# Kernel optimization log

Measured on AMD Instinct MI355X. Metric: run time of the kernel, lower is better.

The kernel has to match this reference:

```python
import jax, jax.numpy as jnp
import numpy as np

N, D_IN, D_OUT, H = 8192, 256, 128, 2
SLOPE = 0.2
EPS = 1e-5  # InstanceNorm2d default eps


def setup_inputs() -> dict:
    key = jax.random.key(0)
    ks = jax.random.split(key, 6)
    x = jax.random.normal(ks[0], (N, D_IN), dtype=jnp.float32)
    conn_mask = jnp.where(jax.random.uniform(ks[1], (N, N)) < 0.05, 0.0, -1e9).astype(jnp.float32)
    W = jax.random.normal(ks[2], (H, D_IN, D_OUT), dtype=jnp.float32) * 0.05
    a_src = jax.random.normal(ks[3], (H, D_OUT), dtype=jnp.float32) * 0.1
    a_tgt = jax.random.normal(ks[4], (H, D_OUT), dtype=jnp.float32) * 0.1
    W_res = jax.random.normal(ks[5], (D_OUT, D_IN), dtype=jnp.float32) * 0.05
    return {"x": x, "conn_mask": conn_mask, "W": W, "a_src": a_src, "a_tgt": a_tgt, "W_res": W_res}


def reference(x, conn_mask, W, a_src, a_tgt, W_res):
    # dropout is identity in eval mode
    proj = jnp.einsum('nd,hdf->hnf', x, W)                      # [H,N,F]
    s_src = jnp.einsum('hnf,hf->hn', proj, a_src)[:, :, None]   # [H,N,1]
    s_tgt = jnp.einsum('hnf,hf->hn', proj, a_tgt)[:, None, :]   # [H,1,N]
    scores = jax.nn.leaky_relu(s_src + s_tgt, negative_slope=SLOPE)  # [H,N,N]
    attn = jax.nn.softmax(conn_mask[None] + scores, axis=1)     # softmax over dim=1 as in torch code
    vals = jnp.einsum('hmn,hnf->hmf', attn, proj)               # bmm -> [H,N,F]
    vals = vals.mean(axis=0)                                    # head mean -> [N,F]
    # InstanceNorm2d(1, affine=False) over the whole [N,F] plane, biased variance
    mu = vals.mean()
    var = jnp.mean(jnp.square(vals - mu))
    vals_norm = (vals - mu) / jnp.sqrt(var + EPS)
    out = vals_norm + x @ W_res.T                               # residual projection (no bias)
    out = jax.nn.elu(out)
    return (out, conn_mask)
```

## Files before the change

kernel.cpp:

```cpp
#include <hip/hip_runtime.h>
#include <stdint.h>

#define NN   8192
#define DIN  256
#define FF   128
#define NF   (NN*FF)
#define SLOPE 0.2f
#define EPSI  1e-5f
#define LOG2E 1.4426950408889634f
#define GEMMB 256

typedef short bf16x8 __attribute__((ext_vector_type(8)));
typedef float f32x4 __attribute__((ext_vector_type(4)));

#define OFF_BM     0
#define OFF_RESID  (2*NF)
#define OFF_AVEC   (3*NF)
#define OFF_SS     (4*NF)
#define OFF_ST     (OFF_SS + 2*NN)
#define OFF_CSUM   (OFF_ST + 2*NN)
#define OFF_STATS  (OFF_CSUM + 2*NN)
#define OFF_NTAB   (OFF_STATS + 16)
#define OFF_VALS   (OFF_NTAB + 4*NN)
#define OFF_WT     (OFF_VALS + NF)
#define OFF_PT2    (OFF_WT + DIN*FF)
#define OFF_VPART  (OFF_PT2 + NF)

__device__ __forceinline__ float lrelu(float x) { return x >= 0.f ? x : SLOPE * x; }

__device__ __forceinline__ float exp2fast(float x) { return __builtin_amdgcn_exp2f(x); }

__device__ __forceinline__ uint32_t bfpack(float a, float b) {
  uint32_t ua = __float_as_uint(a); ua += 0x7fffu + ((ua >> 16) & 1u);
  uint32_t ub = __float_as_uint(b); ub += 0x7fffu + ((ub >> 16) & 1u);
  return (ua >> 16) | (ub & 0xffff0000u);
}

__global__ __launch_bounds__(256) void k_prep(const float* __restrict__ wres, float* __restrict__ wtr,
                                              const float* __restrict__ W, const float* __restrict__ a_src,
                                              const float* __restrict__ a_tgt, float* __restrict__ avec) {
  const int b = blockIdx.x;
  if (b < 128) {
    int i = b * 256 + threadIdx.x;
    int d = i >> 7, f = i & 127;
    wtr[i] = wres[f * DIN + d];
  } else {
    int j = b - 128;
    int h = j & 1, tg = j >> 1;
    const float* a = (tg ? a_tgt : a_src) + h * FF;
    const float* Wp = W + ((size_t)h * DIN + threadIdx.x) * FF;
    float s = 0.f;
#pragma unroll 8
    for (int f = 0; f < FF; ++f) s += Wp[f] * a[f];
    avec[j * DIN + threadIdx.x] = s;
  }
}

__global__ __launch_bounds__(256) void k_ss(const float* __restrict__ x, const float* __restrict__ avec,
                                            float* __restrict__ ss, float* __restrict__ st) {
  const int lane = threadIdx.x & 63, wid = threadIdx.x >> 6;
  const int n = blockIdx.x * 4 + wid;
  float4 xv = *(const float4*)&x[n * DIN + 4 * lane];
  float4 c0 = *(const float4*)&avec[0 * DIN + 4 * lane];
  float4 c1 = *(const float4*)&avec[1 * DIN + 4 * lane];
  float4 c2 = *(const float4*)&avec[2 * DIN + 4 * lane];
  float4 c3 = *(const float4*)&avec[3 * DIN + 4 * lane];
  float v0 = xv.x * c0.x + xv.y * c0.y + xv.z * c0.z + xv.w * c0.w;
  float v1 = xv.x * c1.x + xv.y * c1.y + xv.z * c1.z + xv.w * c1.w;
  float v2 = xv.x * c2.x + xv.y * c2.y + xv.z * c2.z + xv.w * c2.w;
  float v3 = xv.x * c3.x + xv.y * c3.y + xv.z * c3.z + xv.w * c3.w;
#pragma unroll
  for (int o = 1; o < 64; o <<= 1) {
    v0 += __shfl_xor(v0, o); v1 += __shfl_xor(v1, o);
    v2 += __shfl_xor(v2, o); v3 += __shfl_xor(v3, o);
  }
  if (lane == 0) { ss[n] = v0; ss[NN + n] = v1; st[n] = v2; st[NN + n] = v3; }
}

__global__ __launch_bounds__(256) void k_fused(const float* __restrict__ mask, float* __restrict__ maskout,
                                               const float* __restrict__ ss, const float* __restrict__ st,
                                               float* __restrict__ csum, uint32_t* __restrict__ bitmask,
                                               const float* __restrict__ x, const float* __restrict__ Wh,
                                               const float* __restrict__ wtr, uint32_t* __restrict__ pt2,
                                               float* __restrict__ resid) {
  __shared__ float xs[32 * 68];
  __shared__ uint32_t pw[32][129];
  const int b = blockIdx.x;
  const int tid = threadIdx.x;

  if (b >= GEMMB) {
    const int bc = b - GEMMB;
    const int bx = bc & 31, by = bc >> 5;
    const int lane = tid & 63, wv = tid >> 6;
    const int n = bx * 256 + tid;
    const int m0 = by * 128;
    const int wbase = bx * 8 + wv * 2;
    const float st0 = st[n] * LOG2E, st1 = st[NN + n] * LOG2E;
    const float ssA = ss[m0 + lane] * LOG2E,      ssB = ss[m0 + 64 + lane] * LOG2E;
    const float ssC = ss[NN + m0 + lane] * LOG2E, ssD = ss[NN + m0 + 64 + lane] * LOG2E;
    float c0 = 0.f, c1 = 0.f;

    for (int i = 0; i < 128; i += 8) {
      float v[8];
#pragma unroll
      for (int r = 0; r < 8; ++r)
        v[r] = __builtin_nontemporal_load(&mask[(size_t)(m0 + i + r) * NN + n]);
#pragma unroll
      for (int r = 0; r < 8; ++r) {
        const int m = m0 + i + r;
        __builtin_nontemporal_store(v[r], &maskout[(size_t)m * NN + n]);
        bool e = v[r] > -0.5e9f;
        unsigned long long bm = __ballot(e);
        if (lane == 0)
          *(uint2*)&bitmask[m * 256 + wbase] = make_uint2((uint32_t)bm, (uint32_t)(bm >> 32));
        const int ri = i + r;
        float s0 = __uint_as_float(__builtin_amdgcn_readlane(
                     __float_as_uint(ri < 64 ? ssA : ssB), ri & 63));
        float s1 = __uint_as_float(__builtin_amdgcn_readlane(
                     __float_as_uint(ri < 64 ? ssC : ssD), ri & 63));
        float w0 = exp2fast(lrelu(s0 + st0));
        float w1 = exp2fast(lrelu(s1 + st1));
        c0 += e ? w0 : 0.f;
        c1 += e ? w1 : 0.f;
      }
    }
    atomicAdd(&csum[n], c0);
    atomicAdd(&csum[NN + n], c1);
    return;
  }

  const int row0 = b * 32;
  const int ft = tid & 31, rt = tid >> 5;
  const int f0 = ft * 4, r0 = rt * 4;
  float a0[4][4], a1[4][4], a2[4][4];
#pragma unroll
  for (int j = 0; j < 4; ++j)
#pragma unroll
    for (int k = 0; k < 4; ++k) { a0[j][k] = 0.f; a1[j][k] = 0.f; a2[j][k] = 0.f; }

  const float* __restrict__ W0 = Wh;
  const float* __restrict__ W1 = Wh + DIN * FF;

  for (int kc = 0; kc < 4; ++kc) {
    const int d0 = kc * 64;
#pragma unroll
    for (int k2 = 0; k2 < 2; ++k2) {
      int i = tid * 4 + k2 * 1024;
      int r = i >> 6, dd = i & 63;
      *(float4*)&xs[r * 68 + dd] = *(const float4*)&x[(row0 + r) * DIN + d0 + dd];
    }
    __syncthreads();
#pragma unroll
    for (int g = 0; g < 16; ++g) {
      const int dd = g * 4;
      float xr[4][4];
#pragma unroll
      for (int j = 0; j < 4; ++j) {
        float4 t = *(const float4*)&xs[(r0 + j) * 68 + dd];
        xr[j][0] = t.x; xr[j][1] = t.y; xr[j][2] = t.z; xr[j][3] = t.w;
      }
#pragma unroll
      for (int i = 0; i < 4; ++i) {
        const int wrow = (d0 + dd + i) * FF + f0;
        float4 w = *(const float4*)&W0[wrow];
#pragma unroll
        for (int j = 0; j < 4; ++j) {
          float xx = xr[j][i];
          a0[j][0] += xx * w.x; a0[j][1] += xx * w.y; a0[j][2] += xx * w.z; a0[j][3] += xx * w.w;
        }
        w = *(const float4*)&W1[wrow];
#pragma unroll
        for (int j = 0; j < 4; ++j) {
          float xx = xr[j][i];
          a1[j][0] += xx * w.x; a1[j][1] += xx * w.y; a1[j][2] += xx * w.z; a1[j][3] += xx * w.w;
        }
        w = *(const float4*)&wtr[wrow];
#pragma unroll
        for (int j = 0; j < 4; ++j) {
          float xx = xr[j][i];
          a2[j][0] += xx * w.x; a2[j][1] += xx * w.y; a2[j][2] += xx * w.z; a2[j][3] += xx * w.w;
        }
      }
    }
    __syncthreads();
  }

#pragma unroll
  for (int j = 0; j < 4; ++j)
    *(float4*)&resid[(row0 + r0 + j) * FF + f0] = make_float4(a2[j][0], a2[j][1], a2[j][2], a2[j][3]);

#pragma unroll
  for (int j = 0; j < 4; ++j)
#pragma unroll
    for (int k = 0; k < 4; ++k)
      pw[r0 + j][f0 + k] = bfpack(a0[j][k], a1[j][k]);
  __syncthreads();

  const int h = tid >> 7, f = tid & 127;
  uint32_t wbuf[16];
#pragma unroll
  for (int p = 0; p < 16; ++p) {
    uint32_t A = pw[2 * p][f], B = pw[2 * p + 1][f];
    wbuf[p] = h ? ((A >> 16) | (B & 0xffff0000u)) : ((A & 0xffffu) | (B << 16));
  }
  uint32_t* dst = pt2 + ((b * 2 + h) * 128 + f) * 16;
#pragma unroll
  for (int i = 0; i < 4; ++i)
    *(uint4*)&dst[i * 4] = make_uint4(wbuf[i * 4], wbuf[i * 4 + 1], wbuf[i * 4 + 2], wbuf[i * 4 + 3]);
}

__global__ __launch_bounds__(256) void k_ntab(const float* __restrict__ st, const float* __restrict__ csum,
                                              float4* __restrict__ ntab) {
  int i = blockIdx.x * 256 + threadIdx.x;
  ntab[i] = make_float4(st[i] * LOG2E, st[NN + i] * LOG2E, 1.f / csum[i], 1.f / csum[NN + i]);
}

__global__ __launch_bounds__(256) void k_vals(const uint32_t* __restrict__ bitmask, const uint32_t* __restrict__ pt2,
                                              const float4* __restrict__ ntab, const float* __restrict__ ss,
                                              float* __restrict__ vpart) {
  __shared__ short B2[2][8][4][16][8];
  __shared__ short A2[2][8][4][16][8];
  const int t = threadIdx.x;
  const int lane = t & 63, wid = t >> 6;
  const int m0 = blockIdx.x * 128;
  const int nc = blockIdx.y;
  const int q = lane >> 4, col = lane & 15;
  const int n2 = t & 15, mg = t >> 4;
  const int fr = t & 127, hB = t >> 7;

  float ssm0[8], ssm1[8];
#pragma unroll
  for (int p = 0; p < 8; ++p) {
    ssm0[p] = ss[m0 + mg + 16 * p] * LOG2E;
    ssm1[p] = ss[NN + m0 + mg + 16 * p] * LOG2E;
  }

  f32x4 acc[2][8];
#pragma unroll
  for (int i = 0; i < 2; ++i)
#pragma unroll
    for (int j = 0; j < 8; ++j) acc[i][j] = (f32x4){0.f, 0.f, 0.f, 0.f};

  uint32_t* B2w = (uint32_t*)&B2[0][0][0][0][0];
  uint32_t* A2w = (uint32_t*)&A2[0][0][0][0][0];

  for (int s = 0; s < 32; ++s) {
    const int n0 = nc * 1024 + s * 32;
    const uint32_t* src = pt2 + (nc * 32 + s) * 4096;
    {
      const uint4* p4 = (const uint4*)&src[t * 16];
#pragma unroll
      for (int k = 0; k < 4; ++k) {
        uint4 v = p4[k];
        *(uint4*)&B2w[(((hB * 8 + (fr >> 4)) * 4 + k) * 16 + (fr & 15)) * 4] = v;
      }
    }
    float4 na = ntab[n0 + 2 * n2];
    float4 nb = ntab[n0 + 2 * n2 + 1];
#pragma unroll
    for (int p = 0; p < 8; ++p) {
      const int ml = mg + 16 * p;
      uint32_t bw = bitmask[(size_t)(m0 + ml) * 256 + (n0 >> 5)];
      float e0a = exp2fast(lrelu(ssm0[p] + na.x)) * na.z;
      float e1a = exp2fast(lrelu(ssm1[p] + na.y)) * na.w;
      float e0b = exp2fast(lrelu(ssm0[p] + nb.x)) * nb.z;
      float e1b = exp2fast(lrelu(ssm1[p] + nb.y)) * nb.w;
      bool b0 = (bw >> (2 * n2)) & 1, b1 = (bw >> (2 * n2 + 1)) & 1;
      e0a = b0 ? e0a : 0.f; e1a = b0 ? e1a : 0.f;
      e0b = b1 ? e0b : 0.f; e1b = b1 ? e1b : 0.f;
      int base = (p * 4 + (n2 >> 2)) * 64 + mg * 4 + (n2 & 3);
      A2w[base] = bfpack(e0a, e0b);
      A2w[base + 2048] = bfpack(e1a, e1b);
    }
    __syncthreads();
    bf16x8 a00 = *(const bf16x8*)&A2[0][wid * 2][q][col][0];
    bf16x8 a01 = *(const bf16x8*)&A2[0][wid * 2 + 1][q][col][0];
    bf16x8 a10 = *(const bf16x8*)&A2[1][wid * 2][q][col][0];
    bf16x8 a11 = *(const bf16x8*)&A2[1][wid * 2 + 1][q][col][0];
#pragma unroll
    for (int ft = 0; ft < 8; ++ft) {
      bf16x8 b0 = *(const bf16x8*)&B2[0][ft][q][col][0];
      acc[0][ft] = __builtin_amdgcn_mfma_f32_16x16x32_bf16(a00, b0, acc[0][ft], 0, 0, 0);
      acc[1][ft] = __builtin_amdgcn_mfma_f32_16x16x32_bf16(a01, b0, acc[1][ft], 0, 0, 0);
      bf16x8 b1 = *(const bf16x8*)&B2[1][ft][q][col][0];
      acc[0][ft] = __builtin_amdgcn_mfma_f32_16x16x32_bf16(a10, b1, acc[0][ft], 0, 0, 0);
      acc[1][ft] = __builtin_amdgcn_mfma_f32_16x16x32_bf16(a11, b1, acc[1][ft], 0, 0, 0);
    }
    __syncthreads();
  }

  float* dst = vpart + (size_t)nc * NF;
#pragma unroll
  for (int mt2 = 0; mt2 < 2; ++mt2)
#pragma unroll
    for (int ft = 0; ft < 8; ++ft)
#pragma unroll
      for (int r = 0; r < 4; ++r) {
        int mrow = m0 + (wid * 2 + mt2) * 16 + q * 4 + r;
        dst[mrow * FF + ft * 16 + col] = 0.5f * acc[mt2][ft][r];
      }
}

__global__ __launch_bounds__(256) void k_stats(const float* __restrict__ vpart, float* __restrict__ vals,
                                               float* __restrict__ stats) {
  int i = (blockIdx.x * 256 + threadIdx.x) * 4;
  float4 a = make_float4(0.f, 0.f, 0.f, 0.f);
#pragma unroll
  for (int p = 0; p < 8; ++p) {
    float4 v = *(const float4*)&vpart[(size_t)p * NF + i];
    a.x += v.x; a.y += v.y; a.z += v.z; a.w += v.w;
  }
  *(float4*)&vals[i] = a;
  float s = a.x + a.y + a.z + a.w;
  float q = a.x * a.x + a.y * a.y + a.z * a.z + a.w * a.w;
#pragma unroll
  for (int o = 1; o < 64; o <<= 1) { s += __shfl_xor(s, o); q += __shfl_xor(q, o); }
  if ((threadIdx.x & 63) == 0) { atomicAdd(stats, s); atomicAdd(stats + 1, q); }
}

__global__ __launch_bounds__(256) void k_final(const float* __restrict__ vals, const float* __restrict__ resid,
                                               const float* __restrict__ stats, float* __restrict__ out) {
  int i = (blockIdx.x * 256 + threadIdx.x) * 4;
  float mu = stats[0] * (1.f / NF);
  float var = stats[1] * (1.f / NF) - mu * mu;
  float rs = rsqrtf(var + EPSI);
  float4 v = *(const float4*)&vals[i];
  float4 r = *(const float4*)&resid[i];
  float t0 = (v.x - mu) * rs + r.x;
  float t1 = (v.y - mu) * rs + r.y;
  float t2 = (v.z - mu) * rs + r.z;
  float t3 = (v.w - mu) * rs + r.w;
  float4 o;
  o.x = t0 > 0.f ? t0 : expm1f(t0);
  o.y = t1 > 0.f ? t1 : expm1f(t1);
  o.z = t2 > 0.f ? t2 : expm1f(t2);
  o.w = t3 > 0.f ? t3 : expm1f(t3);
  *(float4*)&out[i] = o;
}

extern "C" void kernel_launch(void* const* d_in, const int* in_sizes, int n_in,
                              void* d_out, int out_size, void* d_ws, size_t ws_size,
                              hipStream_t stream) {
  const float* x     = (const float*)d_in[0];
  const float* mask  = (const float*)d_in[1];
  const float* W     = (const float*)d_in[2];
  const float* a_src = (const float*)d_in[3];
  const float* a_tgt = (const float*)d_in[4];
  const float* wres  = (const float*)d_in[5];
  float* out = (float*)d_out;
  float* wsf = (float*)d_ws;

  uint32_t* bitmask = (uint32_t*)(wsf + OFF_BM);
  float*    resid   = wsf + OFF_RESID;
  float*    avec    = wsf + OFF_AVEC;
  float*    ss      = wsf + OFF_SS;
  float*    st      = wsf + OFF_ST;
  float*    csum    = wsf + OFF_CSUM;
  float*    stats   = wsf + OFF_STATS;
  float4*   ntab    = (float4*)(wsf + OFF_NTAB);
  float*    vals    = wsf + OFF_VALS;
  float*    wt      = wsf + OFF_WT;
  uint32_t* pt2     = (uint32_t*)(wsf + OFF_PT2);
  float*    vpart   = wsf + OFF_VPART;

  (void)hipMemsetAsync(csum, 0, (2 * NN + 16) * sizeof(float), stream);

  hipLaunchKernelGGL(k_prep,  dim3(132),           dim3(256), 0, stream, wres, wt, W, a_src, a_tgt, avec);
  hipLaunchKernelGGL(k_ss,    dim3(NN / 4),        dim3(256), 0, stream, x, avec, ss, st);
  hipLaunchKernelGGL(k_fused, dim3(GEMMB + 2048),  dim3(256), 0, stream,
                     mask, out + NF, ss, st, csum, bitmask, x, W, wt, pt2, resid);
  hipLaunchKernelGGL(k_ntab,  dim3(NN / 256),      dim3(256), 0, stream, st, csum, ntab);
  hipLaunchKernelGGL(k_vals,  dim3(NN / 128, 8),   dim3(256), 0, stream, bitmask, pt2, ntab, ss, vpart);
  hipLaunchKernelGGL(k_stats, dim3(NF / 1024),     dim3(256), 0, stream, vpart, vals, stats);
  hipLaunchKernelGGL(k_final, dim3(NF / 1024),     dim3(256), 0, stream, vals, resid, stats, out);
}
```

Baseline: 719.2 us.

## Split fused mask/GEMM kernel into vectorized copy, 3-way GEMM, and bitmask column-sum

Replaces the heterogeneous fused kernel with three kernels. The first is a row-wise float4 mask copy that builds the bitmask through nibble shuffles. The second is a GEMM split across three grid sets (head0, head1, residual) so that it uses more blocks with fewer registers. The third is a separate column-sum kernel that reads the bitmask instead of the float mask and writes ntab directly, which removes the atomics, the csum memset and the k_ntab launch. The aim is better memory coalescing and occupancy. The cost is an extra pass over the bitmask and an extra launch that serializes copy and softmax-denominator work.

```diff
diff --git a/kernel.cpp b/kernel.cpp
--- a/kernel.cpp
+++ b/kernel.cpp
@@ -8,10 +8,10 @@
 #define SLOPE 0.2f
 #define EPSI  1e-5f
 #define LOG2E 1.4426950408889634f
-#define GEMMB 256
 
 typedef short bf16x8 __attribute__((ext_vector_type(8)));
 typedef float f32x4 __attribute__((ext_vector_type(4)));
+typedef float vf4 __attribute__((ext_vector_type(4)));
 
 #define OFF_BM     0
 #define OFF_RESID  (2*NF)
@@ -27,13 +27,41 @@
 #define OFF_VPART  (OFF_PT2 + NF)
 
 __device__ __forceinline__ float lrelu(float x) { return x >= 0.f ? x : SLOPE * x; }
-
 __device__ __forceinline__ float exp2fast(float x) { return __builtin_amdgcn_exp2f(x); }
 
 __device__ __forceinline__ uint32_t bfpack(float a, float b) {
   uint32_t ua = __float_as_uint(a); ua += 0x7fffu + ((ua >> 16) & 1u);
   uint32_t ub = __float_as_uint(b); ub += 0x7fffu + ((ub >> 16) & 1u);
   return (ua >> 16) | (ub & 0xffff0000u);
+}
+__device__ __forceinline__ uint16_t bf16c(float a) {
+  uint32_t u = __float_as_uint(a); u += 0x7fffu + ((u >> 16) & 1u);
+  return (uint16_t)(u >> 16);
+}
+
+__global__ __launch_bounds__(256) void k_copy(const float* __restrict__ mask, float* __restrict__ maskout,
+                                              uint32_t* __restrict__ bitmask) {
+  const int t = threadIdx.x;
+  const int L = t & 63, wv = t >> 6;
+  const int m0 = blockIdx.x * 4;
+#pragma unroll
+  for (int j = 0; j < 4; ++j) {
+    const size_t rowoff = (size_t)(m0 + j) * NN;
+    vf4 v[8];
+#pragma unroll
+    for (int s = 0; s < 8; ++s)
+      v[s] = __builtin_nontemporal_load((const vf4*)&mask[rowoff + s * 1024 + t * 4]);
+#pragma unroll
+    for (int s = 0; s < 8; ++s) {
+      __builtin_nontemporal_store(v[s], (vf4*)&maskout[rowoff + s * 1024 + t * 4]);
+      uint32_t nib = (v[s].x > -0.5e9f ? 1u : 0u) | (v[s].y > -0.5e9f ? 2u : 0u) |
+                     (v[s].z > -0.5e9f ? 4u : 0u) | (v[s].w > -0.5e9f ? 8u : 0u);
+      uint32_t w = nib << (4 * (L & 7));
+      w |= __shfl_xor((int)w, 1); w |= __shfl_xor((int)w, 2); w |= __shfl_xor((int)w, 4);
+      if ((L & 7) == 0)
+        bitmask[(m0 + j) * 256 + s * 32 + wv * 8 + (L >> 3)] = w;
+    }
+  }
 }
 
 __global__ __launch_bounds__(256) void k_prep(const float* __restrict__ wres, float* __restrict__ wtr,
@@ -77,69 +105,23 @@
   if (lane == 0) { ss[n] = v0; ss[NN + n] = v1; st[n] = v2; st[NN + n] = v3; }
 }
 
-__global__ __launch_bounds__(256) void k_fused(const float* __restrict__ mask, float* __restrict__ maskout,
-                                               const float* __restrict__ ss, const float* __restrict__ st,
-                                               float* __restrict__ csum, uint32_t* __restrict__ bitmask,
-                                               const float* __restrict__ x, const float* __restrict__ Wh,
-                                               const float* __restrict__ wtr, uint32_t* __restrict__ pt2,
-                                               float* __restrict__ resid) {
+__global__ __launch_bounds__(256) void k_gemm(const float* __restrict__ x, const float* __restrict__ Wh,
+                                              const float* __restrict__ wtr, uint32_t* __restrict__ pt2,
+                                              float* __restrict__ resid) {
+  const int set = blockIdx.y;
+  const float* __restrict__ Wsrc = (set < 2) ? (Wh + set * (DIN * FF)) : wtr;
+  const int c = blockIdx.x;
+  const int row0 = c * 32;
   __shared__ float xs[32 * 68];
-  __shared__ uint32_t pw[32][129];
-  const int b = blockIdx.x;
+  __shared__ uint16_t pw16[32][132];
   const int tid = threadIdx.x;
-
-  if (b >= GEMMB) {
-    const int bc = b - GEMMB;
-    const int bx = bc & 31, by = bc >> 5;
-    const int lane = tid & 63, wv = tid >> 6;
-    const int n = bx * 256 + tid;
-    const int m0 = by * 128;
-    const int wbase = bx * 8 + wv * 2;
-    const float st0 = st[n] * LOG2E, st1 = st[NN + n] * LOG2E;
-    const float ssA = ss[m0 + lane] * LOG2E,      ssB = ss[m0 + 64 + lane] * LOG2E;
-    const float ssC = ss[NN + m0 + lane] * LOG2E, ssD = ss[NN + m0 + 64 + lane] * LOG2E;
-    float c0 = 0.f, c1 = 0.f;
-
-    for (int i = 0; i < 128; i += 8) {
-      float v[8];
-#pragma unroll
-      for (int r = 0; r < 8; ++r)
-        v[r] = __builtin_nontemporal_load(&mask[(size_t)(m0 + i + r) * NN + n]);
-#pragma unroll
-      for (int r = 0; r < 8; ++r) {
-        const int m = m0 + i + r;
-        __builtin_nontemporal_store(v[r], &maskout[(size_t)m * NN + n]);
-        bool e = v[r] > -0.5e9f;
-        unsigned long long bm = __ballot(e);
-        if (lane == 0)
-          *(uint2*)&bitmask[m * 256 + wbase] = make_uint2((uint32_t)bm, (uint32_t)(bm >> 32));
-        const int ri = i + r;
-        float s0 = __uint_as_float(__builtin_amdgcn_readlane(
-                     __float_as_uint(ri < 64 ? ssA : ssB), ri & 63));
-        float s1 = __uint_as_float(__builtin_amdgcn_readlane(
-                     __float_as_uint(ri < 64 ? ssC : ssD), ri & 63));
-        float w0 = exp2fast(lrelu(s0 + st0));
-        float w1 = exp2fast(lrelu(s1 + st1));
-        c0 += e ? w0 : 0.f;
-        c1 += e ? w1 : 0.f;
-      }
-    }
-    atomicAdd(&csum[n], c0);
-    atomicAdd(&csum[NN + n], c1);
-    return;
-  }
-
-  const int row0 = b * 32;
   const int ft = tid & 31, rt = tid >> 5;
   const int f0 = ft * 4, r0 = rt * 4;
-  float a0[4][4], a1[4][4], a2[4][4];
+  float acc[4][4];
 #pragma unroll
   for (int j = 0; j < 4; ++j)
 #pragma unroll
-    for (int k = 0; k < 4; ++k) { a0[j][k] = 0.f; a1[j][k] = 0.f; a2[j][k] = 0.f; }
-
-  const float* __restrict__ W0 = Wh;
-  const float* __restrict__ W1 = Wh + DIN * FF;
+    for (int k = 0; k < 4; ++k) acc[j][k] = 0.f;
 
   for (int kc = 0; kc < 4; ++kc) {
     const int d0 = kc * 64;
@@ -161,58 +143,73 @@
       }
 #pragma unroll
       for (int i = 0; i < 4; ++i) {
-        const int wrow = (d0 + dd + i) * FF + f0;
-        float4 w = *(const float4*)&W0[wrow];
+        float4 w = *(const float4*)&Wsrc[(d0 + dd + i) * FF + f0];
 #pragma unroll
         for (int j = 0; j < 4; ++j) {
           float xx = xr[j][i];
-          a0[j][0] += xx * w.x; a0[j][1] += xx * w.y; a0[j][2] += xx * w.z; a0[j][3] += xx * w.w;
-        }
-        w = *(const float4*)&W1[wrow];
-#pragma unroll
-        for (int j = 0; j < 4; ++j) {
-          float xx = xr[j][i];
-          a1[j][0] += xx * w.x; a1[j][1] += xx * w.y; a1[j][2] += xx * w.z; a1[j][3] += xx * w.w;
-        }
-        w = *(const float4*)&wtr[wrow];
-#pragma unroll
-        for (int j = 0; j < 4; ++j) {
-          float xx = xr[j][i];
-          a2[j][0] += xx * w.x; a2[j][1] += xx * w.y; a2[j][2] += xx * w.z; a2[j][3] += xx * w.w;
+          acc[j][0] += xx * w.x; acc[j][1] += xx * w.y;
+          acc[j][2] += xx * w.z; acc[j][3] += xx * w.w;
         }
       }
     }
     __syncthreads();
   }
 
+  if (set == 2) {
+#pragma unroll
+    for (int j = 0; j < 4; ++j)
+      *(float4*)&resid[(row0 + r0 + j) * FF + f0] = make_float4(acc[j][0], acc[j][1], acc[j][2], acc[j][3]);
+    return;
+  }
+
 #pragma unroll
   for (int j = 0; j < 4; ++j)
-    *(float4*)&resid[(row0 + r0 + j) * FF + f0] = make_float4(a2[j][0], a2[j][1], a2[j][2], a2[j][3]);
-
-#pragma unroll
-  for (int j = 0; j < 4; ++j)
 #pragma unroll
     for (int k = 0; k < 4; ++k)
-      pw[r0 + j][f0 + k] = bfpack(a0[j][k], a1[j][k]);
+      pw16[r0 + j][f0 + k] = bf16c(acc[j][k]);
   __syncthreads();
 
-  const int h = tid >> 7, f = tid & 127;
-  uint32_t wbuf[16];
-#pragma unroll
-  for (int p = 0; p < 16; ++p) {
-    uint32_t A = pw[2 * p][f], B = pw[2 * p + 1][f];
-    wbuf[p] = h ? ((A >> 16) | (B & 0xffff0000u)) : ((A & 0xffffu) | (B << 16));
-  }
-  uint32_t* dst = pt2 + ((b * 2 + h) * 128 + f) * 16;
-#pragma unroll
-  for (int i = 0; i < 4; ++i)
-    *(uint4*)&dst[i * 4] = make_uint4(wbuf[i * 4], wbuf[i * 4 + 1], wbuf[i * 4 + 2], wbuf[i * 4 + 3]);
-}
-
-__global__ __launch_bounds__(256) void k_ntab(const float* __restrict__ st, const float* __restrict__ csum,
-                                              float4* __restrict__ ntab) {
-  int i = blockIdx.x * 256 + threadIdx.x;
-  ntab[i] = make_float4(st[i] * LOG2E, st[NN + i] * LOG2E, 1.f / csum[i], 1.f / csum[NN + i]);
+  const int half = tid >> 7, f = tid & 127;
+  uint32_t wbuf[8];
+#pragma unroll
+  for (int i = 0; i < 8; ++i) {
+    int p = half * 8 + i;
+    wbuf[i] = (uint32_t)pw16[2 * p][f] | ((uint32_t)pw16[2 * p + 1][f] << 16);
+  }
+  uint32_t* dst = pt2 + ((c * 2 + set) * 128 + f) * 16 + half * 8;
+  *(uint4*)&dst[0] = make_uint4(wbuf[0], wbuf[1], wbuf[2], wbuf[3]);
+  *(uint4*)&dst[4] = make_uint4(wbuf[4], wbuf[5], wbuf[6], wbuf[7]);
+}
+
+__global__ __launch_bounds__(512) void k_csum(const uint32_t* __restrict__ bitmask, const float* __restrict__ ss,
+                                              const float* __restrict__ st, float4* __restrict__ ntab) {
+  __shared__ float red[2][16][32];
+  const int t = threadIdx.x;
+  const int ns = t & 31, slice = t >> 5;
+  const int b = blockIdx.x;
+  const int n = 32 * b + ns;
+  const float st0 = st[n] * LOG2E, st1 = st[NN + n] * LOG2E;
+  float c0 = 0.f, c1 = 0.f;
+#pragma unroll 4
+  for (int mi = 0; mi < 512; ++mi) {
+    const int m = slice * 512 + mi;
+    uint32_t bw = bitmask[m * 256 + b];
+    bool e = (bw >> ns) & 1u;
+    float w0 = exp2fast(lrelu(ss[m] * LOG2E + st0));
+    float w1 = exp2fast(lrelu(ss[NN + m] * LOG2E + st1));
+    c0 += e ? w0 : 0.f;
+    c1 += e ? w1 : 0.f;
+  }
+  red[0][slice][ns] = c0;
+  red[1][slice][ns] = c1;
+  __syncthreads();
+  if (t < 32) {
+    float s0 = 0.f, s1 = 0.f;
+#pragma unroll
+    for (int k = 0; k < 16; ++k) { s0 += red[0][k][t]; s1 += red[1][k][t]; }
+    int nn = 32 * b + t;
+    ntab[nn] = make_float4(st[nn] * LOG2E, st[NN + nn] * LOG2E, 1.f / s0, 1.f / s1);
+  }
 }
 
 __global__ __launch_bounds__(256) void k_vals(const uint32_t* __restrict__ bitmask, const uint32_t* __restrict__ pt2,
@@ -355,7 +352,6 @@
   float*    avec    = wsf + OFF_AVEC;
   float*    ss      = wsf + OFF_SS;
   float*    st      = wsf + OFF_ST;
-  float*    csum    = wsf + OFF_CSUM;
   float*    stats   = wsf + OFF_STATS;
   float4*   ntab    = (float4*)(wsf + OFF_NTAB);
   float*    vals    = wsf + OFF_VALS;
@@ -363,14 +359,14 @@
   uint32_t* pt2     = (uint32_t*)(wsf + OFF_PT2);
   float*    vpart   = wsf + OFF_VPART;
 
-  (void)hipMemsetAsync(csum, 0, (2 * NN + 16) * sizeof(float), stream);
-
-  hipLaunchKernelGGL(k_prep,  dim3(132),           dim3(256), 0, stream, wres, wt, W, a_src, a_tgt, avec);
-  hipLaunchKernelGGL(k_ss,    dim3(NN / 4),        dim3(256), 0, stream, x, avec, ss, st);
-  hipLaunchKernelGGL(k_fused, dim3(GEMMB + 2048),  dim3(256), 0, stream,
-                     mask, out + NF, ss, st, csum, bitmask, x, W, wt, pt2, resid);
-  hipLaunchKernelGGL(k_ntab,  dim3(NN / 256),      dim3(256), 0, stream, st, csum, ntab);
-  hipLaunchKernelGGL(k_vals,  dim3(NN / 128, 8),   dim3(256), 0, stream, bitmask, pt2, ntab, ss, vpart);
-  hipLaunchKernelGGL(k_stats, dim3(NF / 1024),     dim3(256), 0, stream, vpart, vals, stats);
-  hipLaunchKernelGGL(k_final, dim3(NF / 1024),     dim3(256), 0, stream, vals, resid, stats, out);
-}
+  (void)hipMemsetAsync(stats, 0, 16 * sizeof(float), stream);
+
+  hipLaunchKernelGGL(k_copy,  dim3(NN / 4),       dim3(256), 0, stream, mask, out + NF, bitmask);
+  hipLaunchKernelGGL(k_prep,  dim3(132),          dim3(256), 0, stream, wres, wt, W, a_src, a_tgt, avec);
+  hipLaunchKernelGGL(k_ss,    dim3(NN / 4),       dim3(256), 0, stream, x, avec, ss, st);
+  hipLaunchKernelGGL(k_gemm,  dim3(NN / 32, 3),   dim3(256), 0, stream, x, W, wt, pt2, resid);
+  hipLaunchKernelGGL(k_csum,  dim3(NN / 32),      dim3(512), 0, stream, bitmask, ss, st, ntab);
+  hipLaunchKernelGGL(k_vals,  dim3(NN / 128, 8),  dim3(256), 0, stream, bitmask, pt2, ntab, ss, vpart);
+  hipLaunchKernelGGL(k_stats, dim3(NF / 1024),    dim3(256), 0, stream, vpart, vals, stats);
+  hipLaunchKernelGGL(k_final, dim3(NF / 1024),    dim3(256), 0, stream, vals, resid, stats, out);
+}
```

After: 746.3 us. 3.8% more time.
